# Kernel tuning notes

Measured on AMD Instinct MI355X. Metric: run time of the kernel, lower is better.

The kernel has to match this reference:

```python
import jax, jax.numpy as jnp
import numpy as np

H, C = 3, 64          # heads, out_channels
NEG_SLOPE = 0.2       # PyG GATConv leaky_relu default
LN_EPS = 1e-5


def setup_inputs() -> dict:
    key = jax.random.key(0)
    ks = jax.random.split(key, 20)
    N, E, D_in, edge_dim = 50000, 800000, 64, 5
    g = lambda k, shape: (jax.random.normal(k, shape, dtype=jnp.float32) * 0.1)
    return {
        "x": jax.random.normal(ks[0], (N, D_in), dtype=jnp.float32),
        "edge_attr": jax.random.normal(ks[1], (E, edge_dim), dtype=jnp.float32),
        "lin_w": g(ks[2], (D_in, H * C)),          # GATConv.lin (bias=False)
        "att_src": g(ks[3], (H, C)),
        "att_dst": g(ks[4], (H, C)),
        "lin_edge_w": g(ks[5], (edge_dim, H * C)),  # GATConv.lin_edge (bias=False)
        "att_edge": g(ks[6], (H, C)),
        "gat_bias": jnp.zeros((H * C,), jnp.float32),
        "w1": g(ks[7], (H * C, C)),
        "b1": jnp.zeros((C,), jnp.float32),
        "ln1_g": jnp.ones((C,), jnp.float32),
        "ln1_b": jnp.zeros((C,), jnp.float32),
        "w2": g(ks[8], (C, C)),
        "b2": jnp.zeros((C,), jnp.float32),
        "ln2_g": jnp.ones((C,), jnp.float32),
        "ln2_b": jnp.zeros((C,), jnp.float32),
        "edge_index": jax.random.randint(ks[9], (2, E), 0, N),
    }


def layer_norm(x, g, b):
    m = jnp.mean(x, axis=-1, keepdims=True)
    v = jnp.mean((x - m) ** 2, axis=-1, keepdims=True)
    return (x - m) * jax.lax.rsqrt(v + LN_EPS) * g + b


def gat_conv(x, edge_index, edge_attr, lin_w, att_src, att_dst,
             lin_edge_w, att_edge, gat_bias):
    N = x.shape[0]
    src, dst = edge_index[0], edge_index[1]

    # add_self_loops=True with fill_value='mean': self-loop edge_attr is the
    # per-node mean of incoming edge attributes (0 if node has no in-edges).
    attr_sum = jax.ops.segment_sum(edge_attr, dst, num_segments=N)       # [N, edge_dim]
    cnt = jax.ops.segment_sum(jnp.ones((dst.shape[0],), edge_attr.dtype), dst, num_segments=N)
    loop_attr = attr_sum / jnp.maximum(cnt, 1.0)[:, None]
    loop = jnp.arange(N, dtype=src.dtype)
    src = jnp.concatenate([src, loop])
    dst = jnp.concatenate([dst, loop])
    ea = jnp.concatenate([edge_attr, loop_attr], axis=0)                  # [E2, edge_dim]

    xs = (x @ lin_w).reshape(N, H, C)                                     # [N, H, C]
    a_src = jnp.einsum('nhc,hc->nh', xs, att_src)                         # [N, H]
    a_dst = jnp.einsum('nhc,hc->nh', xs, att_dst)                         # [N, H]
    e = (ea @ lin_edge_w).reshape(-1, H, C)                               # [E2, H, C]
    a_edge = jnp.einsum('ehc,hc->eh', e, att_edge)                        # [E2, H]

    logits = a_src[src] + a_dst[dst] + a_edge                             # [E2, H]
    logits = jnp.where(logits >= 0, logits, NEG_SLOPE * logits)           # leaky_relu

    # segment softmax over incoming edges of each dst node (self loops ensure non-empty)
    lmax = jax.ops.segment_max(logits, dst, num_segments=N)               # [N, H]
    ex = jnp.exp(logits - lmax[dst])
    denom = jax.ops.segment_sum(ex, dst, num_segments=N)                  # [N, H]
    alpha = ex / denom[dst]                                               # [E2, H]

    msgs = alpha[:, :, None] * xs[src]                                    # [E2, H, C]
    out = jax.ops.segment_sum(msgs, dst, num_segments=N)                  # [N, H, C]
    return out.reshape(N, H * C) + gat_bias


def reference(x, edge_attr, lin_w, att_src, att_dst, lin_edge_w, att_edge,
              gat_bias, w1, b1, ln1_g, ln1_b, w2, b2, ln2_g, ln2_b, edge_index):
    x_gat = gat_conv(x, edge_index, edge_attr, lin_w, att_src, att_dst,
                     lin_edge_w, att_edge, gat_bias)
    x_gat = x_gat @ w1 + b1                         # linear1: [N, C]
    x_gat = layer_norm(x + x_gat, ln1_g, ln1_b)     # layerNorm1(x + x_gat)
    lin = x_gat @ w2 + b2                           # linear2
    out = layer_norm(lin + x_gat, ln2_g, ln2_b)     # layerNorm2(lin + x_gat)
    return out                                      # dropout p=0 -> identity
```

## Files before the change

### kernel.cpp

```cpp
#include <hip/hip_runtime.h>


#define HH 3
#define CC 64
#define DIN 64
#define ED 5
#define HC 192
#define NEG_SLOPE 0.2f
#define LN_EPS 1e-5f
#define LOG2E 1.44269504f

typedef __attribute__((ext_vector_type(8))) short bf16x8;
typedef __attribute__((ext_vector_type(4))) float f32x4;

__device__ __forceinline__ float leaky(float l) { return fmaxf(l, NEG_SLOPE * l); }

__device__ __forceinline__ unsigned short f2bf(float f) {
    unsigned u = __float_as_uint(f);
    unsigned r = (u + 0x7FFFu + ((u >> 16) & 1u)) >> 16;
    return (unsigned short)r;
}
__device__ __forceinline__ float bf2f(unsigned short u) {
    return __uint_as_float((unsigned)u << 16);
}
__device__ __forceinline__ float bf_lo(unsigned v) { return __uint_as_float(v << 16); }
__device__ __forceinline__ float bf_hi(unsigned v) { return __uint_as_float(v & 0xFFFF0000u); }

__device__ __forceinline__ bf16x8 pack8(float4 a, float4 b) {
    bf16x8 r;
    r[0] = (short)f2bf(a.x); r[1] = (short)f2bf(a.y);
    r[2] = (short)f2bf(a.z); r[3] = (short)f2bf(a.w);
    r[4] = (short)f2bf(b.x); r[5] = (short)f2bf(b.y);
    r[6] = (short)f2bf(b.z); r[7] = (short)f2bf(b.w);
    return r;
}

#define PREP_TOT (HC*DIN + DIN*HC + CC*CC + CC + ED*HH)
#define PREP_BLOCKS 30
__global__ __launch_bounds__(256) void k_prep_cnt(const float* __restrict__ lin_w,
                                                  const float* __restrict__ w1,
                                                  const float* __restrict__ w2,
                                                  const float* __restrict__ b1,
                                                  const float* __restrict__ gat_bias,
                                                  const float* __restrict__ lin_edge_w,
                                                  const float* __restrict__ att_edge,
                                                  unsigned short* __restrict__ linwt,
                                                  unsigned short* __restrict__ w1t,
                                                  unsigned short* __restrict__ w2t,
                                                  float* __restrict__ b1p,
                                                  float* __restrict__ we,
                                                  const int* __restrict__ ei,
                                                  int* __restrict__ icnt, int E) {
    if (blockIdx.x < PREP_BLOCKS) {
        for (int i = blockIdx.x * 256 + threadIdx.x; i < PREP_TOT; i += PREP_BLOCKS * 256) {
            if (i < HC * DIN) {
                int c = i >> 6, k = i & 63;
                linwt[i] = f2bf(lin_w[k * HC + c]);
            } else if (i < 2 * HC * DIN) {
                int j = i - HC * DIN;
                int c = j / HC, k = j - c * HC;
                w1t[j] = f2bf(w1[k * CC + c]);
            } else if (i < 2 * HC * DIN + CC * CC) {
                int j = i - 2 * HC * DIN;
                int c = j >> 6, k = j & 63;
                w2t[j] = f2bf(w2[k * CC + c]);
            } else if (i < 2 * HC * DIN + CC * CC + CC) {
                int c = i - (2 * HC * DIN + CC * CC);
                float s = b1[c];
                for (int k = 0; k < HC; ++k) s += gat_bias[k] * w1[k * CC + c];
                b1p[c] = s;
            } else {
                int q = i - (2 * HC * DIN + CC * CC + CC);
                int d = q / HH, h = q - d * HH;
                float s = 0.f;
                for (int c = 0; c < CC; ++c)
                    s += lin_edge_w[d * HC + h * CC + c] * att_edge[h * CC + c];
                we[q] = s * LOG2E;
            }
        }
    } else {
        int nb = gridDim.x - PREP_BLOCKS;
        for (int e = (blockIdx.x - PREP_BLOCKS) * 256 + threadIdx.x; e < E; e += nb * 256)
            atomicAdd(&icnt[ei[E + e]], 1);
    }
}

__global__ __launch_bounds__(256) void k_xs(const float* __restrict__ x,
                                            const unsigned short* __restrict__ linwt,
                                            const float* __restrict__ att_src,
                                            const float* __restrict__ att_dst,
                                            unsigned short* __restrict__ xsb,
                                            float* __restrict__ a_src,
                                            float* __restrict__ a_dst,
                                            const int* __restrict__ icnt,
                                            int* __restrict__ gtot,
                                            int* __restrict__ off,
                                            int* __restrict__ cursor,
                                            int N, int nbx) {
    __shared__ int wt[4];
    __shared__ int base_sh;
    if ((int)blockIdx.x >= nbx) {
        int bid = blockIdx.x - nbx;
        int i = bid * 256 + threadIdx.x;
        int lane = threadIdx.x & 63, wid = threadIdx.x >> 6;
        int v = (i < N) ? icnt[i] : 0;
        int incl = v;
        #pragma unroll
        for (int o = 1; o < 64; o <<= 1) {
            int u = __shfl_up(incl, o, 64);
            if (lane >= o) incl += u;
        }
        if (lane == 63) wt[wid] = incl;
        __syncthreads();
        if (threadIdx.x == 0)
            base_sh = atomicAdd(gtot, wt[0] + wt[1] + wt[2] + wt[3]);
        __syncthreads();
        int wpre = 0;
        for (int w2 = 0; w2 < wid; ++w2) wpre += wt[w2];
        int excl = base_sh + wpre + incl - v;
        if (i < N) { off[i] = excl; cursor[i] = excl; }
        return;
    }

    int lane = threadIdx.x & 63, w = threadIdx.x >> 6;
    int l15 = lane & 15, kg = (lane >> 4) * 8;
    int nb = blockIdx.x * 64;
    int arow = nb + w * 16 + l15;
    int arow_c = min(arow, N - 1);

    f32x4 acc[12];
    #pragma unroll
    for (int ct = 0; ct < 12; ++ct) acc[ct] = (f32x4){0.f, 0.f, 0.f, 0.f};

    #pragma unroll
    for (int k0 = 0; k0 < DIN; k0 += 32) {
        const float* ap = x + (size_t)arow_c * DIN + k0 + kg;
        float4 a0 = *(const float4*)ap;
        float4 a1 = *(const float4*)(ap + 4);
        bf16x8 af = pack8(a0, a1);
        #pragma unroll
        for (int ct = 0; ct < 12; ++ct) {
            bf16x8 bf = *(const bf16x8*)(linwt + (size_t)(ct * 16 + l15) * DIN + k0 + kg);
            acc[ct] = __builtin_amdgcn_mfma_f32_16x16x32_bf16(af, bf, acc[ct], 0, 0, 0);
        }
    }

    float asv[12], adv[12];
    #pragma unroll
    for (int ct = 0; ct < 12; ++ct) {
        int c = ct * 16 + l15;
        asv[ct] = att_src[c]; adv[ct] = att_dst[c];
    }

    int rbase = nb + w * 16 + (lane >> 4) * 4;
    #pragma unroll
    for (int j = 0; j < 4; ++j) {
        int r = rbase + j;
        bool ok = r < N;
        float ps0 = 0.f, ps1 = 0.f, ps2 = 0.f, pd0 = 0.f, pd1 = 0.f, pd2 = 0.f;
        #pragma unroll
        for (int ct = 0; ct < 12; ++ct) {
            float v = acc[ct][j];
            float s = v * asv[ct], d = v * adv[ct];
            if (ct < 4)      { ps0 += s; pd0 += d; }
            else if (ct < 8) { ps1 += s; pd1 += d; }
            else             { ps2 += s; pd2 += d; }
        }
        if (ok) {
            unsigned* row32 = (unsigned*)(xsb + (size_t)r * HC);
            #pragma unroll
            for (int ct = 0; ct < 4; ++ct) {
                int c = ct * 16 + l15;
                row32[c] = (unsigned)f2bf(acc[ct][j]) | ((unsigned)f2bf(acc[ct + 4][j]) << 16);
                xsb[(size_t)r * HC + 128 + c] = f2bf(acc[ct + 8][j]);
            }
        }
        #pragma unroll
        for (int o = 1; o < 16; o <<= 1) {
            ps0 += __shfl_xor(ps0, o, 64); pd0 += __shfl_xor(pd0, o, 64);
            ps1 += __shfl_xor(ps1, o, 64); pd1 += __shfl_xor(pd1, o, 64);
            ps2 += __shfl_xor(ps2, o, 64); pd2 += __shfl_xor(pd2, o, 64);
        }
        if (ok && l15 == 0) {
            a_src[r * HH + 0] = ps0 * LOG2E; a_src[r * HH + 1] = ps1 * LOG2E;
            a_src[r * HH + 2] = ps2 * LOG2E;
            a_dst[r * HH + 0] = pd0 * LOG2E; a_dst[r * HH + 1] = pd1 * LOG2E;
            a_dst[r * HH + 2] = pd2 * LOG2E;
        }
    }
}

__global__ __launch_bounds__(256) void k_fill(const float* __restrict__ ea,
                                              const int* __restrict__ ei,
                                              const float* __restrict__ a_src,
                                              const float* __restrict__ a_dst,
                                              const float* __restrict__ we,
                                              int* __restrict__ cursor,
                                              uint4* __restrict__ payload, int E) {
    int e = blockIdx.x * blockDim.x + threadIdx.x;
    if (e >= E) return;
    int s = ei[e], d = ei[E + e];
    int pos = atomicAdd(&cursor[d], 1);
    float attr[ED];
    #pragma unroll
    for (int j = 0; j < ED; ++j) attr[j] = ea[(size_t)e * ED + j];
    float aeh[HH], lp[HH];
    #pragma unroll
    for (int h = 0; h < HH; ++h) {
        float a = 0.f;
        #pragma unroll
        for (int j = 0; j < ED; ++j) a += attr[j] * we[j * HH + h];
        aeh[h] = a;
        lp[h] = a_src[s * HH + h] + a_dst[d * HH + h] + a;
    }
    uint4 pk;
    pk.x = (unsigned)f2bf(lp[0])  | ((unsigned)f2bf(lp[1])  << 16);
    pk.y = (unsigned)f2bf(lp[2])  | ((unsigned)f2bf(aeh[0]) << 16);
    pk.z = (unsigned)f2bf(aeh[1]) | ((unsigned)f2bf(aeh[2]) << 16);
    pk.w = (unsigned)s;
    payload[pos] = pk;
}

__global__ __launch_bounds__(256) void k_gatmlp(const unsigned short* __restrict__ xsb,
                                                const float* __restrict__ a_src,
                                                const float* __restrict__ a_dst,
                                                const int* __restrict__ off,
                                                const int* __restrict__ icnt,
                                                const uint4* __restrict__ payload,
                                                const float* __restrict__ x,
                                                const unsigned short* __restrict__ w1t,
                                                const unsigned short* __restrict__ w2t,
                                                const float* __restrict__ b1p,
                                                const float* __restrict__ g1,
                                                const float* __restrict__ be1,
                                                const float* __restrict__ b2,
                                                const float* __restrict__ g2,
                                                const float* __restrict__ be2,
                                                float* __restrict__ out, int N) {
    __shared__ float4 wbuf[4][64];
    __shared__ unsigned short OA[16 * HC];
    __shared__ unsigned short H1s[16 * 72];
    __shared__ float red[2][4][16];
    int lane = threadIdx.x & 63;
    int wid  = threadIdx.x >> 6;
    const unsigned* xs32 = (const unsigned*)xsb;
    unsigned c128ml = 128u - (unsigned)lane;
    int nb16 = blockIdx.x * 16;

    #pragma unroll 1
    for (int t = 0; t < 4; ++t) {
        int row = wid * 4 + t;
        int n = nb16 + row;
        if (n < N) {
            int beg = off[n];
            int deg = icnt[n];
            float pden0 = 0.f, pden1 = 0.f, pden2 = 0.f;
            float pae0 = 0.f, pae1 = 0.f, pae2 = 0.f;
            float a0A = 0.f, a1A = 0.f, a2A = 0.f;
            float a0B = 0.f, a1B = 0.f, a2B = 0.f;

            for (int c0 = 0; c0 < deg; c0 += 64) {
                int cn = min(deg - c0, 64);
                float w0 = 0.f, w1 = 0.f, w2 = 0.f;
                int src = 0;
                if (lane < cn) {
                    uint4 p = payload[beg + c0 + lane];
                    w0 = exp2f(leaky(bf_lo(p.x)));
                    w1 = exp2f(leaky(bf_hi(p.x)));
                    w2 = exp2f(leaky(bf_lo(p.y)));
                    pae0 += bf_hi(p.y);
                    pae1 += bf_lo(p.z);
                    pae2 += bf_hi(p.z);
                    pden0 += w0; pden1 += w1; pden2 += w2;
                    src = (int)p.w;
                }
                wbuf[wid][lane] = make_float4(w0, w1, w2, __int_as_float(src));
                int i = 0;
                for (; i + 2 <= cn; i += 2) {
                    float4 ta = wbuf[wid][i];
                    float4 tb = wbuf[wid][i + 1];
                    unsigned ia = __umul24((unsigned)__float_as_int(ta.w), 96u) + lane;
                    unsigned ib = __umul24((unsigned)__float_as_int(tb.w), 96u) + lane;
                    unsigned va = xs32[ia];
                    unsigned vb = xs32[ib];
                    float xa2 = bf2f(xsb[(ia << 1) + c128ml]);
                    float xb2 = bf2f(xsb[(ib << 1) + c128ml]);
                    a0A += ta.x * bf_lo(va); a1A += ta.y * bf_hi(va); a2A += ta.z * xa2;
                    a0B += tb.x * bf_lo(vb); a1B += tb.y * bf_hi(vb); a2B += tb.z * xb2;
                }
                if (i < cn) {
                    float4 ta = wbuf[wid][i];
                    unsigned ia = __umul24((unsigned)__float_as_int(ta.w), 96u) + lane;
                    unsigned va = xs32[ia];
                    a0A += ta.x * bf_lo(va);
                    a1A += ta.y * bf_hi(va);
                    a2A += ta.z * bf2f(xsb[(ia << 1) + c128ml]);
                }
            }

            #pragma unroll
            for (int o = 32; o; o >>= 1) {
                pden0 += __shfl_xor(pden0, o, 64);
                pden1 += __shfl_xor(pden1, o, 64);
                pden2 += __shfl_xor(pden2, o, 64);
                pae0  += __shfl_xor(pae0, o, 64);
                pae1  += __shfl_xor(pae1, o, 64);
                pae2  += __shfl_xor(pae2, o, 64);
            }

            float dc = fmaxf((float)deg, 1.0f);
            float inv_dc = __builtin_amdgcn_rcpf(dc);
            float sl0 = leaky(a_src[n * HH + 0] + a_dst[n * HH + 0] + pae0 * inv_dc);
            float sl1 = leaky(a_src[n * HH + 1] + a_dst[n * HH + 1] + pae1 * inv_dc);
            float sl2 = leaky(a_src[n * HH + 2] + a_dst[n * HH + 2] + pae2 * inv_dc);
            float e0 = exp2f(sl0), e1 = exp2f(sl1), e2 = exp2f(sl2);
            unsigned ian = __umul24((unsigned)n, 96u) + lane;
            unsigned van = xs32[ian];
            float xn2 = bf2f(xsb[(ian << 1) + c128ml]);
            float r0 = __builtin_amdgcn_rcpf(pden0 + e0);
            float r1 = __builtin_amdgcn_rcpf(pden1 + e1);
            float r2 = __builtin_amdgcn_rcpf(pden2 + e2);
            OA[row * HC +       lane] = f2bf((a0A + a0B + e0 * bf_lo(van)) * r0);
            OA[row * HC +  64 + lane] = f2bf((a1A + a1B + e1 * bf_hi(van)) * r1);
            OA[row * HC + 128 + lane] = f2bf((a2A + a2B + e2 * xn2) * r2);
        } else {
            OA[row * HC +       lane] = 0;
            OA[row * HC +  64 + lane] = 0;
            OA[row * HC + 128 + lane] = 0;
        }
    }
    __syncthreads();

    int l15 = lane & 15, kg = (lane >> 4) * 8;
    int col = wid * 16 + l15;
    float cb1 = b1p[col], cg1 = g1[col], cbe1 = be1[col];
    float cb2 = b2[col],  cg2 = g2[col], cbe2 = be2[col];

    f32x4 acc = (f32x4){0.f, 0.f, 0.f, 0.f};
    #pragma unroll
    for (int k0 = 0; k0 < HC; k0 += 32) {
        bf16x8 af = *(const bf16x8*)&OA[l15 * HC + k0 + kg];
        bf16x8 bf = *(const bf16x8*)(w1t + (size_t)col * HC + k0 + kg);
        acc = __builtin_amdgcn_mfma_f32_16x16x32_bf16(af, bf, acc, 0, 0, 0);
    }

    int rj0 = (lane >> 4) * 4;
    float y[4], h1v[4];
    #pragma unroll
    for (int j = 0; j < 4; ++j) {
        int r = min(nb16 + rj0 + j, N - 1);
        y[j] = acc[j] + cb1 + x[(size_t)r * DIN + col];
        float s = y[j], q = y[j] * y[j];
        #pragma unroll
        for (int o = 1; o < 16; o <<= 1) {
            s += __shfl_xor(s, o, 64);
            q += __shfl_xor(q, o, 64);
        }
        if (l15 == 0) { red[0][wid][rj0 + j] = s; red[1][wid][rj0 + j] = q; }
    }
    __syncthreads();
    #pragma unroll
    for (int j = 0; j < 4; ++j) {
        int rj = rj0 + j;
        float s = red[0][0][rj] + red[0][1][rj] + red[0][2][rj] + red[0][3][rj];
        float q = red[1][0][rj] + red[1][1][rj] + red[1][2][rj] + red[1][3][rj];
        float m = s * (1.0f / CC);
        float var = q * (1.0f / CC) - m * m;
        float inv = rsqrtf(var + LN_EPS);
        float h = (y[j] - m) * inv * cg1 + cbe1;
        h1v[j] = h;
        H1s[rj * 72 + col] = f2bf(h);
    }
    __syncthreads();

    f32x4 acc2 = (f32x4){0.f, 0.f, 0.f, 0.f};
    #pragma unroll
    for (int k0 = 0; k0 < CC; k0 += 32) {
        bf16x8 af = *(const bf16x8*)&H1s[l15 * 72 + k0 + kg];
        bf16x8 bf = *(const bf16x8*)(w2t + (size_t)col * CC + k0 + kg);
        acc2 = __builtin_amdgcn_mfma_f32_16x16x32_bf16(af, bf, acc2, 0, 0, 0);
    }

    float z[4];
    #pragma unroll
    for (int j = 0; j < 4; ++j) {
        z[j] = acc2[j] + cb2 + h1v[j];
        float s = z[j], q = z[j] * z[j];
        #pragma unroll
        for (int o = 1; o < 16; o <<= 1) {
            s += __shfl_xor(s, o, 64);
            q += __shfl_xor(q, o, 64);
        }
        if (l15 == 0) { red[0][wid][rj0 + j] = s; red[1][wid][rj0 + j] = q; }
    }
    __syncthreads();
    #pragma unroll
    for (int j = 0; j < 4; ++j) {
        int rj = rj0 + j;
        float s = red[0][0][rj] + red[0][1][rj] + red[0][2][rj] + red[0][3][rj];
        float q = red[1][0][rj] + red[1][1][rj] + red[1][2][rj] + red[1][3][rj];
        float m = s * (1.0f / CC);
        float var = q * (1.0f / CC) - m * m;
        float inv = rsqrtf(var + LN_EPS);
        int r = nb16 + rj;
        if (r < N)
            out[(size_t)r * CC + col] = (z[j] - m) * inv * cg2 + cbe2;
    }
}

extern "C" void kernel_launch(void* const* d_in, const int* in_sizes, int n_in,
                              void* d_out, int out_size, void* d_ws, size_t ws_size,
                              hipStream_t stream) {
    const float* x          = (const float*)d_in[0];
    const float* edge_attr  = (const float*)d_in[1];
    const float* lin_w      = (const float*)d_in[2];
    const float* att_src    = (const float*)d_in[3];
    const float* att_dst    = (const float*)d_in[4];
    const float* lin_edge_w = (const float*)d_in[5];
    const float* att_edge   = (const float*)d_in[6];
    const float* gat_bias   = (const float*)d_in[7];
    const float* w1         = (const float*)d_in[8];
    const float* b1         = (const float*)d_in[9];
    const float* ln1_g      = (const float*)d_in[10];
    const float* ln1_b      = (const float*)d_in[11];
    const float* w2         = (const float*)d_in[12];
    const float* b2         = (const float*)d_in[13];
    const float* ln2_g      = (const float*)d_in[14];
    const float* ln2_b      = (const float*)d_in[15];
    const int*   ei         = (const int*)d_in[16];
    float* out = (float*)d_out;

    const int N = in_sizes[0] / DIN;
    const int E = in_sizes[1] / ED;
    const int nb_scan = (N + 255) / 256;
    const int nbx = (N + 63) / 64;

    char* ws = (char*)d_ws;
    size_t off_b = 0;
    auto alloc = [&](size_t bytes) {
        size_t o = off_b;
        off_b = (off_b + bytes + 255) & ~(size_t)255;
        return o;
    };
    int* icnt = (int*)(ws + alloc((size_t)N * 4));
    int* gtot = (int*)(ws + alloc(4));
    size_t zero_bytes = off_b;
    unsigned short* xsb = (unsigned short*)(ws + alloc((size_t)N * HC * 2));
    float*  a_srcb  = (float*)(ws + alloc((size_t)N * HH * 4));
    float*  a_dstb  = (float*)(ws + alloc((size_t)N * HH * 4));
    int*    offb    = (int*)(ws + alloc((size_t)N * 4));
    int*    cursor  = (int*)(ws + alloc((size_t)N * 4));
    uint4*  payload = (uint4*)(ws + alloc((size_t)E * 16));
    unsigned short* linwt = (unsigned short*)(ws + alloc((size_t)HC * DIN * 2));
    unsigned short* w1t   = (unsigned short*)(ws + alloc((size_t)DIN * HC * 2));
    unsigned short* w2t   = (unsigned short*)(ws + alloc((size_t)CC * CC * 2));
    float* b1p = (float*)(ws + alloc((size_t)CC * 4));
    float* we  = (float*)(ws + alloc((size_t)ED * HH * 4));
    (void)ws_size; (void)n_in; (void)out_size;

    hipMemsetAsync(d_ws, 0, zero_bytes, stream);

    k_prep_cnt<<<PREP_BLOCKS + (E + 255) / 256, 256, 0, stream>>>(
        lin_w, w1, w2, b1, gat_bias, lin_edge_w, att_edge,
        linwt, w1t, w2t, b1p, we, ei, icnt, E);
    k_xs<<<nbx + nb_scan, 256, 0, stream>>>(x, linwt, att_src, att_dst, xsb,
                                            a_srcb, a_dstb, icnt, gtot, offb, cursor,
                                            N, nbx);
    k_fill<<<(E + 255) / 256, 256, 0, stream>>>(edge_attr, ei, a_srcb, a_dstb, we, cursor,
                                                payload, E);
    k_gatmlp<<<(N + 15) / 16, 256, 0, stream>>>(xsb, a_srcb, a_dstb, offb, icnt, payload,
                                                x, w1t, w2t, b1p, ln1_g, ln1_b,
                                                b2, ln2_g, ln2_b, out, N);
}
```

Before: 184.1 us.

## Process four destination nodes per wave concurrently with 16-lane edge groups

Restructures the GAT aggregation so each wave handles its four destination nodes together: each 16-lane group loads and scores edges for one node, instead of looping over the nodes one at a time with 64-lane edge chunks. This cuts the serial per-node loop and the wasted lanes when a node has far fewer than 64 edges (average degree is about 16). The shared-memory OA row stride is also padded to 200 to reduce bank conflicts in the MFMA operand reads. The cost is more register pressure from per-node accumulators, and the loop runs to the largest degree among the four nodes.

```diff
diff --git a/kernel.cpp b/kernel.cpp
--- a/kernel.cpp
+++ b/kernel.cpp
@@ -6,6 +6,7 @@
 #define DIN 64
 #define ED 5
 #define HC 192
+#define OAP 200
 #define NEG_SLOPE 0.2f
 #define LN_EPS 1e-5f
 #define LOG2E 1.44269504f
@@ -238,7 +239,7 @@
                                                 const float* __restrict__ be2,
                                                 float* __restrict__ out, int N) {
     __shared__ float4 wbuf[4][64];
-    __shared__ unsigned short OA[16 * HC];
+    __shared__ unsigned short OA[16 * OAP];
     __shared__ unsigned short H1s[16 * 72];
     __shared__ float red[2][4][16];
     int lane = threadIdx.x & 63;
@@ -247,87 +248,101 @@
     unsigned c128ml = 128u - (unsigned)lane;
     int nb16 = blockIdx.x * 16;
 
-    #pragma unroll 1
-    for (int t = 0; t < 4; ++t) {
-        int row = wid * 4 + t;
-        int n = nb16 + row;
-        if (n < N) {
-            int beg = off[n];
-            int deg = icnt[n];
-            float pden0 = 0.f, pden1 = 0.f, pden2 = 0.f;
-            float pae0 = 0.f, pae1 = 0.f, pae2 = 0.f;
-            float a0A = 0.f, a1A = 0.f, a2A = 0.f;
-            float a0B = 0.f, a1B = 0.f, a2B = 0.f;
-
-            for (int c0 = 0; c0 < deg; c0 += 64) {
-                int cn = min(deg - c0, 64);
-                float w0 = 0.f, w1 = 0.f, w2 = 0.f;
-                int src = 0;
-                if (lane < cn) {
-                    uint4 p = payload[beg + c0 + lane];
-                    w0 = exp2f(leaky(bf_lo(p.x)));
-                    w1 = exp2f(leaky(bf_hi(p.x)));
-                    w2 = exp2f(leaky(bf_lo(p.y)));
-                    pae0 += bf_hi(p.y);
-                    pae1 += bf_lo(p.z);
-                    pae2 += bf_hi(p.z);
-                    pden0 += w0; pden1 += w1; pden2 += w2;
-                    src = (int)p.w;
-                }
-                wbuf[wid][lane] = make_float4(w0, w1, w2, __int_as_float(src));
-                int i = 0;
-                for (; i + 2 <= cn; i += 2) {
-                    float4 ta = wbuf[wid][i];
-                    float4 tb = wbuf[wid][i + 1];
-                    unsigned ia = __umul24((unsigned)__float_as_int(ta.w), 96u) + lane;
-                    unsigned ib = __umul24((unsigned)__float_as_int(tb.w), 96u) + lane;
-                    unsigned va = xs32[ia];
-                    unsigned vb = xs32[ib];
-                    float xa2 = bf2f(xsb[(ia << 1) + c128ml]);
-                    float xb2 = bf2f(xsb[(ib << 1) + c128ml]);
-                    a0A += ta.x * bf_lo(va); a1A += ta.y * bf_hi(va); a2A += ta.z * xa2;
-                    a0B += tb.x * bf_lo(vb); a1B += tb.y * bf_hi(vb); a2B += tb.z * xb2;
-                }
-                if (i < cn) {
-                    float4 ta = wbuf[wid][i];
-                    unsigned ia = __umul24((unsigned)__float_as_int(ta.w), 96u) + lane;
-                    unsigned va = xs32[ia];
-                    a0A += ta.x * bf_lo(va);
-                    a1A += ta.y * bf_hi(va);
-                    a2A += ta.z * bf2f(xsb[(ia << 1) + c128ml]);
-                }
+    int ngrp = lane >> 4, eslot = lane & 15;
+    int n_g = nb16 + wid * 4 + ngrp;
+    int n_gc = min(n_g, N - 1);
+    int beg_g = off[n_gc];
+    int deg_g = (n_g < N) ? icnt[n_g] : 0;
+
+    int maxdeg = deg_g;
+    maxdeg = max(maxdeg, __shfl_xor(maxdeg, 16, 64));
+    maxdeg = max(maxdeg, __shfl_xor(maxdeg, 32, 64));
+
+    float pden0 = 0.f, pden1 = 0.f, pden2 = 0.f;
+    float pae0 = 0.f, pae1 = 0.f, pae2 = 0.f;
+    float aA0[4], aA1[4], aA2[4], aB0[4], aB1[4], aB2[4];
+    #pragma unroll
+    for (int g = 0; g < 4; ++g) {
+        aA0[g] = 0.f; aA1[g] = 0.f; aA2[g] = 0.f;
+        aB0[g] = 0.f; aB1[g] = 0.f; aB2[g] = 0.f;
+    }
+
+    for (int c0 = 0; c0 < maxdeg; c0 += 16) {
+        float w0 = 0.f, w1 = 0.f, w2 = 0.f;
+        int src = 0;
+        if (c0 + eslot < deg_g) {
+            uint4 p = payload[beg_g + c0 + eslot];
+            w0 = exp2f(leaky(bf_lo(p.x)));
+            w1 = exp2f(leaky(bf_hi(p.x)));
+            w2 = exp2f(leaky(bf_lo(p.y)));
+            pae0 += bf_hi(p.y);
+            pae1 += bf_lo(p.z);
+            pae2 += bf_hi(p.z);
+            pden0 += w0; pden1 += w1; pden2 += w2;
+            src = (int)p.w;
+        }
+        wbuf[wid][lane] = make_float4(w0, w1, w2, __int_as_float(src));
+        #pragma unroll
+        for (int g = 0; g < 4; ++g) {
+            int dg = __shfl(deg_g, g * 16, 64);
+            int cn = min(dg - c0, 16);
+            int i = 0;
+            for (; i + 2 <= cn; i += 2) {
+                float4 ta = wbuf[wid][g * 16 + i];
+                float4 tb = wbuf[wid][g * 16 + i + 1];
+                unsigned ia = __umul24((unsigned)__float_as_int(ta.w), 96u) + lane;
+                unsigned ib = __umul24((unsigned)__float_as_int(tb.w), 96u) + lane;
+                unsigned va = xs32[ia];
+                unsigned vb = xs32[ib];
+                float xa2 = bf2f(xsb[(ia << 1) + c128ml]);
+                float xb2 = bf2f(xsb[(ib << 1) + c128ml]);
+                aA0[g] += ta.x * bf_lo(va); aA1[g] += ta.y * bf_hi(va); aA2[g] += ta.z * xa2;
+                aB0[g] += tb.x * bf_lo(vb); aB1[g] += tb.y * bf_hi(vb); aB2[g] += tb.z * xb2;
             }
-
-            #pragma unroll
-            for (int o = 32; o; o >>= 1) {
-                pden0 += __shfl_xor(pden0, o, 64);
-                pden1 += __shfl_xor(pden1, o, 64);
-                pden2 += __shfl_xor(pden2, o, 64);
-                pae0  += __shfl_xor(pae0, o, 64);
-                pae1  += __shfl_xor(pae1, o, 64);
-                pae2  += __shfl_xor(pae2, o, 64);
+            if (i < cn) {
+                float4 ta = wbuf[wid][g * 16 + i];
+                unsigned ia = __umul24((unsigned)__float_as_int(ta.w), 96u) + lane;
+                unsigned va = xs32[ia];
+                aA0[g] += ta.x * bf_lo(va);
+                aA1[g] += ta.y * bf_hi(va);
+                aA2[g] += ta.z * bf2f(xsb[(ia << 1) + c128ml]);
             }
-
-            float dc = fmaxf((float)deg, 1.0f);
-            float inv_dc = __builtin_amdgcn_rcpf(dc);
-            float sl0 = leaky(a_src[n * HH + 0] + a_dst[n * HH + 0] + pae0 * inv_dc);
-            float sl1 = leaky(a_src[n * HH + 1] + a_dst[n * HH + 1] + pae1 * inv_dc);
-            float sl2 = leaky(a_src[n * HH + 2] + a_dst[n * HH + 2] + pae2 * inv_dc);
-            float e0 = exp2f(sl0), e1 = exp2f(sl1), e2 = exp2f(sl2);
-            unsigned ian = __umul24((unsigned)n, 96u) + lane;
-            unsigned van = xs32[ian];
-            float xn2 = bf2f(xsb[(ian << 1) + c128ml]);
-            float r0 = __builtin_amdgcn_rcpf(pden0 + e0);
-            float r1 = __builtin_amdgcn_rcpf(pden1 + e1);
-            float r2 = __builtin_amdgcn_rcpf(pden2 + e2);
-            OA[row * HC +       lane] = f2bf((a0A + a0B + e0 * bf_lo(van)) * r0);
-            OA[row * HC +  64 + lane] = f2bf((a1A + a1B + e1 * bf_hi(van)) * r1);
-            OA[row * HC + 128 + lane] = f2bf((a2A + a2B + e2 * xn2) * r2);
-        } else {
-            OA[row * HC +       lane] = 0;
-            OA[row * HC +  64 + lane] = 0;
-            OA[row * HC + 128 + lane] = 0;
-        }
+        }
+    }
+
+    #pragma unroll
+    for (int o = 1; o < 16; o <<= 1) {
+        pden0 += __shfl_xor(pden0, o, 64);
+        pden1 += __shfl_xor(pden1, o, 64);
+        pden2 += __shfl_xor(pden2, o, 64);
+        pae0  += __shfl_xor(pae0, o, 64);
+        pae1  += __shfl_xor(pae1, o, 64);
+        pae2  += __shfl_xor(pae2, o, 64);
+    }
+
+    float dc = fmaxf((float)deg_g, 1.0f);
+    float inv_dc = __builtin_amdgcn_rcpf(dc);
+    int nh = n_gc * HH;
+    float sl0 = leaky(a_src[nh + 0] + a_dst[nh + 0] + pae0 * inv_dc);
+    float sl1 = leaky(a_src[nh + 1] + a_dst[nh + 1] + pae1 * inv_dc);
+    float sl2 = leaky(a_src[nh + 2] + a_dst[nh + 2] + pae2 * inv_dc);
+    float e0 = exp2f(sl0), e1 = exp2f(sl1), e2 = exp2f(sl2);
+    float r0 = __builtin_amdgcn_rcpf(pden0 + e0);
+    float r1 = __builtin_amdgcn_rcpf(pden1 + e1);
+    float r2 = __builtin_amdgcn_rcpf(pden2 + e2);
+
+    #pragma unroll
+    for (int g = 0; g < 4; ++g) {
+        int row = wid * 4 + g;
+        int n2c = min(nb16 + row, N - 1);
+        float e0g = __shfl(e0, g * 16, 64), e1g = __shfl(e1, g * 16, 64), e2g = __shfl(e2, g * 16, 64);
+        float r0g = __shfl(r0, g * 16, 64), r1g = __shfl(r1, g * 16, 64), r2g = __shfl(r2, g * 16, 64);
+        unsigned ian = __umul24((unsigned)n2c, 96u) + lane;
+        unsigned van = xs32[ian];
+        float xn2v = bf2f(xsb[(ian << 1) + c128ml]);
+        OA[row * OAP +       lane] = f2bf((aA0[g] + aB0[g] + e0g * bf_lo(van)) * r0g);
+        OA[row * OAP +  64 + lane] = f2bf((aA1[g] + aB1[g] + e1g * bf_hi(van)) * r1g);
+        OA[row * OAP + 128 + lane] = f2bf((aA2[g] + aB2[g] + e2g * xn2v) * r2g);
     }
     __syncthreads();
 
@@ -339,7 +354,7 @@
     f32x4 acc = (f32x4){0.f, 0.f, 0.f, 0.f};
     #pragma unroll
     for (int k0 = 0; k0 < HC; k0 += 32) {
-        bf16x8 af = *(const bf16x8*)&OA[l15 * HC + k0 + kg];
+        bf16x8 af = *(const bf16x8*)&OA[l15 * OAP + k0 + kg];
         bf16x8 bf = *(const bf16x8*)(w1t + (size_t)col * HC + k0 + kg);
         acc = __builtin_amdgcn_mfma_f32_16x16x32_bf16(af, bf, acc, 0, 0, 0);
     }
```

New measurement: 188.1 us. +2.2%, slower.
